# Performance work log

Hardware: AMD Instinct MI355X
Metric: run time of the kernel (lower is better)

## Reference

```python
import jax, jax.numpy as jnp
import numpy as np

C = 128          # inchannel
CH = C // 2      # projected channels
N_, D_, H_, W_ = 2, 16, 16, 16


def setup_inputs() -> dict:
    key = jax.random.key(0)
    kx, kq, kk, kv, kp = jax.random.split(key, 5)
    s_in = 1.0 / np.sqrt(C)
    s_mid = 1.0 / np.sqrt(CH)
    return {
        "x": jax.random.normal(kx, (N_, C, D_, H_, W_), dtype=jnp.float32),
        "Wq": jax.random.normal(kq, (CH, C), dtype=jnp.float32) * s_in,
        "Wk": jax.random.normal(kk, (CH, C), dtype=jnp.float32) * s_in,
        "Wv": jax.random.normal(kv, (CH, C), dtype=jnp.float32) * s_in,
        "Wpost": jax.random.normal(kp, (C, CH), dtype=jnp.float32) * s_mid,
    }


def reference(x, Wq, Wk, Wv, Wpost):
    n, c_in, d, h, w = x.shape
    npos = d * h * w
    xf = x.reshape(n, c_in, npos)                     # (n, C, N)
    # 1x1x1 conv3d (no bias) == channel-mixing matmul
    q = jnp.einsum('oc,ncx->nox', Wq, xf)             # (n, CH, N)
    k = jnp.einsum('oc,ncx->nox', Wk, xf)             # (n, CH, N)
    v = jnp.einsum('oc,ncx->nox', Wv, xf)             # (n, CH, N)
    # atten_map[b,i,j] = sum_c k[b,c,i] * q[b,c,j], softmax over j (dim=2)
    scores = jnp.einsum('nci,ncj->nij', k, q)         # (n, N, N)
    attn = jax.nn.softmax(scores, axis=2)
    # val @ attn: out[b,c,j] = sum_i v[b,c,i] * attn[b,i,j]
    agg = jnp.einsum('nci,nij->ncj', v, attn)         # (n, CH, N)
    post = jnp.einsum('oc,ncx->nox', Wpost, agg)      # (n, C, N)
    return post.reshape(n, c_in, d, h, w) + x
```

## Files before the change

kernel.cpp:

```cpp
#include <hip/hip_runtime.h>
#include <math.h>

#define NB   2
#define CIN  128
#define CH   64
#define NPOS 4096

typedef __attribute__((ext_vector_type(8))) short s16x8;
typedef __attribute__((ext_vector_type(4))) float f32x4;

__device__ __forceinline__ unsigned int bfrne(float f) {
    unsigned int u = __float_as_uint(f);
    return (u + 0x7FFFu + ((u >> 16) & 1u)) >> 16;
}
__device__ __forceinline__ unsigned int pk_rne(float lo, float hi) {
    return bfrne(lo) | (bfrne(hi) << 16);
}
__device__ __forceinline__ unsigned int pk_fast(float lo, float hi) {
    unsigned int a = (__float_as_uint(lo) + 0x8000u) >> 16;
    unsigned int b = (__float_as_uint(hi) + 0x8000u) & 0xFFFF0000u;
    return a | b;
}
__device__ __forceinline__ float bf2f(unsigned short h) {
    return __uint_as_float(((unsigned int)h) << 16);
}

__global__ __launch_bounds__(256) void packw_kernel(
    const float* __restrict__ Wq, const float* __restrict__ Wk,
    const float* __restrict__ Wv, const float* __restrict__ Wpost,
    unsigned short* __restrict__ Wb)
{
    const int gid = blockIdx.x * 256 + threadIdx.x;
    const int base = gid * 4;
    const int mat = base >> 13, off = base & 8191;
    const float* src = (mat == 0) ? Wq : (mat == 1) ? Wk : (mat == 2) ? Wv : Wpost;
    float4 f = *(const float4*)&src[off];
    uint2 st = make_uint2(pk_rne(f.x, f.y), pk_rne(f.z, f.w));
    *(uint2*)&Wb[mat * 8192 + off] = st;
}

#define XTS 132
__global__ __launch_bounds__(256) void qkv_kernel(
    const float* __restrict__ x, const unsigned short* __restrict__ Wb,
    unsigned short* __restrict__ kT, unsigned short* __restrict__ qT,
    float* __restrict__ v32)
{
    __shared__ __align__(16) float xT[16 * XTS];
    const int b  = blockIdx.y;
    const int p0 = blockIdx.x * 16;
    const int tid = threadIdx.x;

    #pragma unroll
    for (int it = 0; it < 2; ++it) {
        int idx = it * 256 + tid;
        int c = idx >> 2, p4 = (idx & 3) * 4;
        float4 g = *(const float4*)&x[((size_t)b * CIN + c) * NPOS + p0 + p4];
        xT[(p4 + 0) * XTS + c] = g.x;
        xT[(p4 + 1) * XTS + c] = g.y;
        xT[(p4 + 2) * XTS + c] = g.z;
        xT[(p4 + 3) * XTS + c] = g.w;
    }
    __syncthreads();

    const int w = tid >> 6, l = tid & 63, lm = l & 15, lq = l >> 4;
    const int p = p0 + lm;

    s16x8 Bhi[4], Blo[4];
    #pragma unroll
    for (int ck = 0; ck < 4; ++ck) {
        const float* xr = &xT[lm * XTS + ck * 32 + lq * 8];
        union { unsigned int u[4]; s16x8 v; } chv, clv;
        #pragma unroll
        for (int j = 0; j < 4; ++j) {
            float x0 = xr[2 * j], x1 = xr[2 * j + 1];
            unsigned int h0 = bfrne(x0), h1 = bfrne(x1);
            chv.u[j] = h0 | (h1 << 16);
            clv.u[j] = pk_rne(x0 - __uint_as_float(h0 << 16),
                              x1 - __uint_as_float(h1 << 16));
        }
        Bhi[ck] = chv.v; Blo[ck] = clv.v;
    }

    #pragma unroll
    for (int t3 = 0; t3 < 3; ++t3) {
        const int tile = w * 3 + t3;
        const int mat = tile >> 2, o0 = (tile & 3) * 16;
        const unsigned short* Wm = Wb + mat * 8192;
        f32x4 acc = {0.f, 0.f, 0.f, 0.f};
        #pragma unroll
        for (int ck = 0; ck < 4; ++ck) {
            s16x8 aW = *(const s16x8*)&Wm[(o0 + lm) * CIN + ck * 32 + lq * 8];
            acc = __builtin_amdgcn_mfma_f32_16x16x32_bf16(aW, Bhi[ck], acc, 0,0,0);
            acc = __builtin_amdgcn_mfma_f32_16x16x32_bf16(aW, Blo[ck], acc, 0,0,0);
        }
        if (mat < 2) {
            unsigned short* dst = (mat == 0) ? qT : kT;
            uint2 st = make_uint2(pk_rne(acc[0], acc[1]), pk_rne(acc[2], acc[3]));
            *(uint2*)&dst[((size_t)b * NPOS + p) * CH + o0 + lq * 4] = st;
        } else {
            #pragma unroll
            for (int r = 0; r < 4; ++r)
                v32[((size_t)b * CH + o0 + lq * 4 + r) * NPOS + p] = acc[r];
        }
    }
}

__global__ __launch_bounds__(256) void stats_kernel(
    const unsigned short* __restrict__ kT,
    const unsigned short* __restrict__ qT,
    float* __restrict__ lpart)
{
    __shared__ __align__(16) unsigned short qbuf[4096];
    const int b  = blockIdx.z;
    const int jq = blockIdx.y;
    const int i0 = blockIdx.x * 128;
    const int tid = threadIdx.x;
    const int w = tid >> 6, l = tid & 63, lm = l & 15, lq = l >> 4;

    s16x8 a[2][2];
    #pragma unroll
    for (int s = 0; s < 2; ++s)
        #pragma unroll
        for (int kc = 0; kc < 2; ++kc)
            a[s][kc] = *(const s16x8*)&kT[
                ((size_t)b * NPOS + i0 + w * 32 + s * 16 + lm) * CH + kc * 32 + lq * 8];

    const unsigned short* qpt =
        qT + ((size_t)b * NPOS + jq * 512 + w * 16 + lm) * CH + lq * 8;
    s16x8 st0 = *(const s16x8*)(qpt);
    s16x8 st1 = *(const s16x8*)(qpt + 32);

    float rs[2][4] = {};
    for (int t = 0; t < 8; ++t) {
        *(s16x8*)&qbuf[(2 * w + 0) * 512 + l * 8] = st0;
        *(s16x8*)&qbuf[(2 * w + 1) * 512 + l * 8] = st1;
        __syncthreads();
        if (t < 7) {
            const unsigned short* qn = qpt + (size_t)(t + 1) * 64 * CH;
            st0 = *(const s16x8*)(qn);
            st1 = *(const s16x8*)(qn + 32);
        }
        #pragma unroll
        for (int js = 0; js < 4; ++js) {
            s16x8 b0 = *(const s16x8*)&qbuf[(js * 2 + 0) * 512 + l * 8];
            s16x8 b1 = *(const s16x8*)&qbuf[(js * 2 + 1) * 512 + l * 8];
            #pragma unroll
            for (int s = 0; s < 2; ++s) {
                f32x4 sc = {0.f, 0.f, 0.f, 0.f};
                sc = __builtin_amdgcn_mfma_f32_16x16x32_bf16(a[s][0], b0, sc, 0,0,0);
                sc = __builtin_amdgcn_mfma_f32_16x16x32_bf16(a[s][1], b1, sc, 0,0,0);
                rs[s][0] += __expf(sc[0]); rs[s][1] += __expf(sc[1]);
                rs[s][2] += __expf(sc[2]); rs[s][3] += __expf(sc[3]);
            }
        }
        __syncthreads();
    }

    #pragma unroll
    for (int s = 0; s < 2; ++s)
        #pragma unroll
        for (int r = 0; r < 4; ++r) {
            #pragma unroll
            for (int m = 1; m < 16; m <<= 1)
                rs[s][r] += __shfl_xor(rs[s][r], m);
        }
    if (lm == 0) {
        #pragma unroll
        for (int s = 0; s < 2; ++s)
            #pragma unroll
            for (int r = 0; r < 4; ++r)
                lpart[(size_t)jq * NB * NPOS + b * NPOS
                      + i0 + w * 32 + s * 16 + lq * 4 + r] = rs[s][r];
    }
}

__global__ __launch_bounds__(256) void combine_kernel(
    const float* __restrict__ lpart, const float* __restrict__ v32,
    unsigned short* __restrict__ vbs)
{
    const int idx4 = blockIdx.x * 256 + threadIdx.x;
    const int base = idx4 * 4;
    const int b = base >> 18;
    const int i = base & (NPOS - 1);
    const float* lp = lpart + b * NPOS + i;
    float sx = 0.f, sy = 0.f, sz = 0.f, sw = 0.f;
    #pragma unroll
    for (int qq = 0; qq < 8; ++qq) {
        float4 lv = *(const float4*)(lp + (size_t)qq * NB * NPOS);
        sx += lv.x; sy += lv.y; sz += lv.z; sw += lv.w;
    }
    float4 v = *(const float4*)&v32[base];
    uint2 st = make_uint2(pk_rne(v.x / sx, v.y / sy),
                          pk_rne(v.z / sz, v.w / sw));
    *(uint2*)&vbs[base] = st;
}

__global__ __launch_bounds__(256) void agg_kernel(
    const unsigned short* __restrict__ kT,
    const unsigned short* __restrict__ qT,
    const unsigned short* __restrict__ vbs,
    unsigned short* __restrict__ U)
{
    __shared__ __align__(16) unsigned short kbuf[2048];
    __shared__ __align__(16) unsigned short vbuf[2048];
    const int b  = blockIdx.z;
    const int iq = blockIdx.y;
    const int j0 = blockIdx.x * 128;
    const int tid = threadIdx.x;
    const int w = tid >> 6, l = tid & 63, lm = l & 15, lq = l >> 4;

    s16x8 qb[2][2];
    #pragma unroll
    for (int js = 0; js < 2; ++js)
        #pragma unroll
        for (int kc = 0; kc < 2; ++kc)
            qb[js][kc] = *(const s16x8*)&qT[
                ((size_t)b * NPOS + j0 + w * 32 + js * 16 + lm) * CH + kc * 32 + lq * 8];

    int addr[4];
    #pragma unroll
    for (int d = 0; d < 4; ++d)
        addr[d] = (lm + 16 * (2 * (lq & 1) + (d >> 1))) << 2;
    const bool lowhalf = (lq < 2);

    const unsigned short* kpt = kT
        + ((size_t)b * NPOS + iq * 512 + (w >> 1) * 16 + lm) * CH
        + (w & 1) * 32 + lq * 8;
    const unsigned short* vpt = vbs
        + ((size_t)b * CH + w * 16 + lm) * NPOS + iq * 512 + lq * 8;

    f32x4 acc[2][4] = {};
    s16x8 kst = *(const s16x8*)kpt;
    s16x8 vst = *(const s16x8*)vpt;

    for (int t = 0; t < 16; ++t) {
        *(s16x8*)&kbuf[w * 512 + l * 8] = kst;
        *(s16x8*)&vbuf[w * 512 + l * 8] = vst;
        __syncthreads();
        if (t < 15) {
            kst = *(const s16x8*)(kpt + (t + 1) * 32 * CH);
            vst = *(const s16x8*)(vpt + (t + 1) * 32);
        }
        s16x8 kA[2][2], vA[4];
        #pragma unroll
        for (int s = 0; s < 2; ++s)
            #pragma unroll
            for (int kc = 0; kc < 2; ++kc)
                kA[s][kc] = *(const s16x8*)&kbuf[(s * 2 + kc) * 512 + l * 8];
        #pragma unroll
        for (int cs = 0; cs < 4; ++cs)
            vA[cs] = *(const s16x8*)&vbuf[cs * 512 + l * 8];

        #pragma unroll
        for (int js = 0; js < 2; ++js) {
            f32x4 s0 = {0,0,0,0}, s1 = {0,0,0,0};
            s0 = __builtin_amdgcn_mfma_f32_16x16x32_bf16(kA[0][0], qb[js][0], s0, 0,0,0);
            s0 = __builtin_amdgcn_mfma_f32_16x16x32_bf16(kA[0][1], qb[js][1], s0, 0,0,0);
            s1 = __builtin_amdgcn_mfma_f32_16x16x32_bf16(kA[1][0], qb[js][0], s1, 0,0,0);
            s1 = __builtin_amdgcn_mfma_f32_16x16x32_bf16(kA[1][1], qb[js][1], s1, 0,0,0);

            unsigned int P0[2], P1[2];
            P0[0] = pk_fast(__expf(s0[0]), __expf(s0[1]));
            P0[1] = pk_fast(__expf(s0[2]), __expf(s0[3]));
            P1[0] = pk_fast(__expf(s1[0]), __expf(s1[1]));
            P1[1] = pk_fast(__expf(s1[2]), __expf(s1[3]));

            union { unsigned int u[4]; s16x8 v; } B;
            #pragma unroll
            for (int d = 0; d < 4; ++d) {
                int t0 = __builtin_amdgcn_ds_bpermute(addr[d], (int)P0[d & 1]);
                int t1 = __builtin_amdgcn_ds_bpermute(addr[d], (int)P1[d & 1]);
                B.u[d] = lowhalf ? (unsigned int)t0 : (unsigned int)t1;
            }
            #pragma unroll
            for (int cs = 0; cs < 4; ++cs)
                acc[js][cs] = __builtin_amdgcn_mfma_f32_16x16x32_bf16(
                    vA[cs], B.v, acc[js][cs], 0,0,0);
        }
        __syncthreads();
    }

    unsigned short* Up = U + ((size_t)iq * NB + b) * NPOS * CH;
    #pragma unroll
    for (int js = 0; js < 2; ++js)
        #pragma unroll
        for (int cs = 0; cs < 4; ++cs) {
            uint2 st = make_uint2(pk_rne(acc[js][cs][0], acc[js][cs][1]),
                                  pk_rne(acc[js][cs][2], acc[js][cs][3]));
            *(uint2*)&Up[(size_t)(j0 + w * 32 + js * 16 + lm) * CH
                         + cs * 16 + lq * 4] = st;
        }
}

__global__ __launch_bounds__(256) void post_kernel(
    const float* __restrict__ x, const unsigned short* __restrict__ Wb,
    const unsigned short* __restrict__ U, float* __restrict__ out)
{
    const int b  = blockIdx.y;
    const int p0 = blockIdx.x * 32;
    const int tid = threadIdx.x;
    const int w = tid >> 6, l = tid & 63, lm = l & 15, lq = l >> 4;
    const int psub = (w & 1) * 16, ohalf = w >> 1;
    const int p = p0 + psub + lm;
    const size_t PS = (size_t)NB * NPOS * CH;

    const unsigned short* u = U + ((size_t)b * NPOS + p) * CH;
    const unsigned short* Wpb = Wb + 3 * 8192;
    s16x8 Bf[2];
    #pragma unroll
    for (int ck = 0; ck < 2; ++ck) {
        float sv[8] = {};
        #pragma unroll
        for (int qq = 0; qq < 8; ++qq) {
            union { s16x8 v; unsigned short us[8]; } uu;
            uu.v = *(const s16x8*)(u + (size_t)qq * PS + ck * 32 + lq * 8);
            #pragma unroll
            for (int j = 0; j < 8; ++j) sv[j] += bf2f(uu.us[j]);
        }
        union { unsigned int u[4]; s16x8 v; } cb;
        #pragma unroll
        for (int j = 0; j < 4; ++j) cb.u[j] = pk_rne(sv[2*j], sv[2*j+1]);
        Bf[ck] = cb.v;
    }

    #pragma unroll
    for (int ot = 0; ot < 4; ++ot) {
        const int o0 = (ohalf * 4 + ot) * 16;
        f32x4 acc = {0.f, 0.f, 0.f, 0.f};
        #pragma unroll
        for (int ck = 0; ck < 2; ++ck) {
            s16x8 aW = *(const s16x8*)&Wpb[(o0 + lm) * CH + ck * 32 + lq * 8];
            acc = __builtin_amdgcn_mfma_f32_16x16x32_bf16(aW, Bf[ck], acc, 0,0,0);
        }
        #pragma unroll
        for (int r = 0; r < 4; ++r) {
            size_t gi = ((size_t)b * CIN + o0 + lq * 4 + r) * NPOS + p;
            out[gi] = x[gi] + acc[r];
        }
    }
}

extern "C" void kernel_launch(void* const* d_in, const int* in_sizes, int n_in,
                              void* d_out, int out_size, void* d_ws, size_t ws_size,
                              hipStream_t stream) {
    const float* x     = (const float*)d_in[0];
    const float* Wq    = (const float*)d_in[1];
    const float* Wk    = (const float*)d_in[2];
    const float* Wv    = (const float*)d_in[3];
    const float* Wpost = (const float*)d_in[4];
    float* out = (float*)d_out;

    unsigned short* kT  = (unsigned short*)d_ws;
    unsigned short* qT  = kT + (size_t)NB * NPOS * CH;
    unsigned short* vbs = qT + (size_t)NB * NPOS * CH;
    unsigned short* Wb  = vbs + (size_t)NB * NPOS * CH;
    float* lpart = (float*)(Wb + 4 * 8192);
    unsigned short* U = (unsigned short*)(lpart + (size_t)8 * NB * NPOS);
    float* v32 = (float*)U;

    packw_kernel  <<<dim3(32), 256, 0, stream>>>(Wq, Wk, Wv, Wpost, Wb);
    qkv_kernel    <<<dim3(NPOS / 16, NB), 256, 0, stream>>>(x, Wb, kT, qT, v32);
    stats_kernel  <<<dim3(NPOS / 128, 8, NB), 256, 0, stream>>>(kT, qT, lpart);
    combine_kernel<<<dim3(NB * CH * NPOS / 1024), 256, 0, stream>>>(lpart, v32, vbs);
    agg_kernel    <<<dim3(NPOS / 128, 8, NB), 256, 0, stream>>>(kT, qT, vbs, U);
    post_kernel   <<<dim3(NPOS / 32, NB), 256, 0, stream>>>(x, Wb, U, out);
}
```

Before: 109.9 us.

## Split kernels into finer grids and double-buffer LDS tiles in attention passes

The change splits every stage into more blocks. qkv gets a third grid axis over output-tile groups, stats uses 64-row key blocks, agg splits the key range into 16 partials instead of 8, and post handles 16 positions and sums 16 partials. The stats and agg loops now use two LDS buffers, so one __syncthreads per iteration can be removed, and launch bounds request 4 blocks per CU. The aim is better occupancy and more blocks across the CUs. In exchange, post reads twice as many partial buffers, the U workspace grows, and qkv recomputes the x transpose once per output group.

Measured after the change: 118.5 us. 7.9% more time.

```diff
diff --git a/kernel.cpp b/kernel.cpp
--- a/kernel.cpp
+++ b/kernel.cpp
@@ -40,13 +40,14 @@
 }
 
 #define XTS 132
-__global__ __launch_bounds__(256) void qkv_kernel(
+__global__ __launch_bounds__(256, 4) void qkv_kernel(
     const float* __restrict__ x, const unsigned short* __restrict__ Wb,
     unsigned short* __restrict__ kT, unsigned short* __restrict__ qT,
     float* __restrict__ v32)
 {
     __shared__ __align__(16) float xT[16 * XTS];
-    const int b  = blockIdx.y;
+    const int b  = blockIdx.z;
+    const int og = blockIdx.y;
     const int p0 = blockIdx.x * 16;
     const int tid = threadIdx.x;
 
@@ -81,96 +82,84 @@
         Bhi[ck] = chv.v; Blo[ck] = clv.v;
     }
 
-    #pragma unroll
-    for (int t3 = 0; t3 < 3; ++t3) {
-        const int tile = w * 3 + t3;
-        const int mat = tile >> 2, o0 = (tile & 3) * 16;
-        const unsigned short* Wm = Wb + mat * 8192;
-        f32x4 acc = {0.f, 0.f, 0.f, 0.f};
-        #pragma unroll
-        for (int ck = 0; ck < 4; ++ck) {
-            s16x8 aW = *(const s16x8*)&Wm[(o0 + lm) * CIN + ck * 32 + lq * 8];
-            acc = __builtin_amdgcn_mfma_f32_16x16x32_bf16(aW, Bhi[ck], acc, 0,0,0);
-            acc = __builtin_amdgcn_mfma_f32_16x16x32_bf16(aW, Blo[ck], acc, 0,0,0);
-        }
-        if (mat < 2) {
-            unsigned short* dst = (mat == 0) ? qT : kT;
-            uint2 st = make_uint2(pk_rne(acc[0], acc[1]), pk_rne(acc[2], acc[3]));
-            *(uint2*)&dst[((size_t)b * NPOS + p) * CH + o0 + lq * 4] = st;
-        } else {
-            #pragma unroll
-            for (int r = 0; r < 4; ++r)
-                v32[((size_t)b * CH + o0 + lq * 4 + r) * NPOS + p] = acc[r];
-        }
-    }
-}
-
-__global__ __launch_bounds__(256) void stats_kernel(
+    const int tile = og * 4 + w;
+    const int mat = tile >> 2, o0 = (tile & 3) * 16;
+    const unsigned short* Wm = Wb + mat * 8192;
+    f32x4 acc = {0.f, 0.f, 0.f, 0.f};
+    #pragma unroll
+    for (int ck = 0; ck < 4; ++ck) {
+        s16x8 aW = *(const s16x8*)&Wm[(o0 + lm) * CIN + ck * 32 + lq * 8];
+        acc = __builtin_amdgcn_mfma_f32_16x16x32_bf16(aW, Bhi[ck], acc, 0,0,0);
+        acc = __builtin_amdgcn_mfma_f32_16x16x32_bf16(aW, Blo[ck], acc, 0,0,0);
+    }
+    if (mat < 2) {
+        unsigned short* dst = (mat == 0) ? qT : kT;
+        uint2 st = make_uint2(pk_rne(acc[0], acc[1]), pk_rne(acc[2], acc[3]));
+        *(uint2*)&dst[((size_t)b * NPOS + p) * CH + o0 + lq * 4] = st;
+    } else {
+        #pragma unroll
+        for (int r = 0; r < 4; ++r)
+            v32[((size_t)b * CH + o0 + lq * 4 + r) * NPOS + p] = acc[r];
+    }
+}
+
+__global__ __launch_bounds__(256, 4) void stats_kernel(
     const unsigned short* __restrict__ kT,
     const unsigned short* __restrict__ qT,
     float* __restrict__ lpart)
 {
-    __shared__ __align__(16) unsigned short qbuf[4096];
+    __shared__ __align__(16) unsigned short qbuf[2][4096];
     const int b  = blockIdx.z;
     const int jq = blockIdx.y;
-    const int i0 = blockIdx.x * 128;
+    const int i0 = blockIdx.x * 64;
     const int tid = threadIdx.x;
     const int w = tid >> 6, l = tid & 63, lm = l & 15, lq = l >> 4;
 
-    s16x8 a[2][2];
-    #pragma unroll
-    for (int s = 0; s < 2; ++s)
-        #pragma unroll
-        for (int kc = 0; kc < 2; ++kc)
-            a[s][kc] = *(const s16x8*)&kT[
-                ((size_t)b * NPOS + i0 + w * 32 + s * 16 + lm) * CH + kc * 32 + lq * 8];
+    s16x8 a0 = *(const s16x8*)&kT[
+        ((size_t)b * NPOS + i0 + w * 16 + lm) * CH + lq * 8];
+    s16x8 a1 = *(const s16x8*)&kT[
+        ((size_t)b * NPOS + i0 + w * 16 + lm) * CH + 32 + lq * 8];
 
     const unsigned short* qpt =
         qT + ((size_t)b * NPOS + jq * 512 + w * 16 + lm) * CH + lq * 8;
     s16x8 st0 = *(const s16x8*)(qpt);
     s16x8 st1 = *(const s16x8*)(qpt + 32);
 
-    float rs[2][4] = {};
+    float rs[4] = {0.f, 0.f, 0.f, 0.f};
     for (int t = 0; t < 8; ++t) {
-        *(s16x8*)&qbuf[(2 * w + 0) * 512 + l * 8] = st0;
-        *(s16x8*)&qbuf[(2 * w + 1) * 512 + l * 8] = st1;
-        __syncthreads();
+        const int buf = t & 1;
+        *(s16x8*)&qbuf[buf][(2 * w + 0) * 512 + l * 8] = st0;
+        *(s16x8*)&qbuf[buf][(2 * w + 1) * 512 + l * 8] = st1;
         if (t < 7) {
             const unsigned short* qn = qpt + (size_t)(t + 1) * 64 * CH;
             st0 = *(const s16x8*)(qn);
             st1 = *(const s16x8*)(qn + 32);
         }
+        __syncthreads();
         #pragma unroll
         for (int js = 0; js < 4; ++js) {
-            s16x8 b0 = *(const s16x8*)&qbuf[(js * 2 + 0) * 512 + l * 8];
-            s16x8 b1 = *(const s16x8*)&qbuf[(js * 2 + 1) * 512 + l * 8];
-            #pragma unroll
-            for (int s = 0; s < 2; ++s) {
-                f32x4 sc = {0.f, 0.f, 0.f, 0.f};
-                sc = __builtin_amdgcn_mfma_f32_16x16x32_bf16(a[s][0], b0, sc, 0,0,0);
-                sc = __builtin_amdgcn_mfma_f32_16x16x32_bf16(a[s][1], b1, sc, 0,0,0);
-                rs[s][0] += __expf(sc[0]); rs[s][1] += __expf(sc[1]);
-                rs[s][2] += __expf(sc[2]); rs[s][3] += __expf(sc[3]);
-            }
-        }
-        __syncthreads();
-    }
-
-    #pragma unroll
-    for (int s = 0; s < 2; ++s)
-        #pragma unroll
-        for (int r = 0; r < 4; ++r) {
-            #pragma unroll
-            for (int m = 1; m < 16; m <<= 1)
-                rs[s][r] += __shfl_xor(rs[s][r], m);
-        }
+            s16x8 b0 = *(const s16x8*)&qbuf[buf][(js * 2 + 0) * 512 + l * 8];
+            s16x8 b1 = *(const s16x8*)&qbuf[buf][(js * 2 + 1) * 512 + l * 8];
+            f32x4 sc = {0.f, 0.f, 0.f, 0.f};
+            sc = __builtin_amdgcn_mfma_f32_16x16x32_bf16(a0, b0, sc, 0,0,0);
+            sc = __builtin_amdgcn_mfma_f32_16x16x32_bf16(a1, b1, sc, 0,0,0);
+            rs[0] += __expf(sc[0]); rs[1] += __expf(sc[1]);
+            rs[2] += __expf(sc[2]); rs[3] += __expf(sc[3]);
+        }
+    }
+
+    #pragma unroll
+    for (int r = 0; r < 4; ++r) {
+        rs[r] += __shfl_xor(rs[r], 1);
+        rs[r] += __shfl_xor(rs[r], 2);
+        rs[r] += __shfl_xor(rs[r], 4);
+        rs[r] += __shfl_xor(rs[r], 8);
+    }
     if (lm == 0) {
         #pragma unroll
-        for (int s = 0; s < 2; ++s)
-            #pragma unroll
-            for (int r = 0; r < 4; ++r)
-                lpart[(size_t)jq * NB * NPOS + b * NPOS
-                      + i0 + w * 32 + s * 16 + lq * 4 + r] = rs[s][r];
+        for (int r = 0; r < 4; ++r)
+            lpart[(size_t)jq * NB * NPOS + b * NPOS
+                  + i0 + w * 16 + lq * 4 + r] = rs[r];
     }
 }
 
@@ -195,14 +184,14 @@
     *(uint2*)&vbs[base] = st;
 }
 
-__global__ __launch_bounds__(256) void agg_kernel(
+__global__ __launch_bounds__(256, 4) void agg_kernel(
     const unsigned short* __restrict__ kT,
     const unsigned short* __restrict__ qT,
     const unsigned short* __restrict__ vbs,
     unsigned short* __restrict__ U)
 {
-    __shared__ __align__(16) unsigned short kbuf[2048];
-    __shared__ __align__(16) unsigned short vbuf[2048];
+    __shared__ __align__(16) unsigned short kbuf[2][2048];
+    __shared__ __align__(16) unsigned short vbuf[2][2048];
     const int b  = blockIdx.z;
     const int iq = blockIdx.y;
     const int j0 = blockIdx.x * 128;
@@ -224,32 +213,34 @@
     const bool lowhalf = (lq < 2);
 
     const unsigned short* kpt = kT
-        + ((size_t)b * NPOS + iq * 512 + (w >> 1) * 16 + lm) * CH
+        + ((size_t)b * NPOS + iq * 256 + (w >> 1) * 16 + lm) * CH
         + (w & 1) * 32 + lq * 8;
     const unsigned short* vpt = vbs
-        + ((size_t)b * CH + w * 16 + lm) * NPOS + iq * 512 + lq * 8;
+        + ((size_t)b * CH + w * 16 + lm) * NPOS + iq * 256 + lq * 8;
 
     f32x4 acc[2][4] = {};
     s16x8 kst = *(const s16x8*)kpt;
     s16x8 vst = *(const s16x8*)vpt;
 
-    for (int t = 0; t < 16; ++t) {
-        *(s16x8*)&kbuf[w * 512 + l * 8] = kst;
-        *(s16x8*)&vbuf[w * 512 + l * 8] = vst;
-        __syncthreads();
-        if (t < 15) {
+    for (int t = 0; t < 8; ++t) {
+        const int buf = t & 1;
+        *(s16x8*)&kbuf[buf][w * 512 + l * 8] = kst;
+        *(s16x8*)&vbuf[buf][w * 512 + l * 8] = vst;
+        if (t < 7) {
             kst = *(const s16x8*)(kpt + (t + 1) * 32 * CH);
             vst = *(const s16x8*)(vpt + (t + 1) * 32);
         }
+        __syncthreads();
+
         s16x8 kA[2][2], vA[4];
         #pragma unroll
         for (int s = 0; s < 2; ++s)
             #pragma unroll
             for (int kc = 0; kc < 2; ++kc)
-                kA[s][kc] = *(const s16x8*)&kbuf[(s * 2 + kc) * 512 + l * 8];
+                kA[s][kc] = *(const s16x8*)&kbuf[buf][(s * 2 + kc) * 512 + l * 8];
         #pragma unroll
         for (int cs = 0; cs < 4; ++cs)
-            vA[cs] = *(const s16x8*)&vbuf[cs * 512 + l * 8];
+            vA[cs] = *(const s16x8*)&vbuf[buf][cs * 512 + l * 8];
 
         #pragma unroll
         for (int js = 0; js < 2; ++js) {
@@ -277,7 +268,6 @@
                 acc[js][cs] = __builtin_amdgcn_mfma_f32_16x16x32_bf16(
                     vA[cs], B.v, acc[js][cs], 0,0,0);
         }
-        __syncthreads();
     }
 
     unsigned short* Up = U + ((size_t)iq * NB + b) * NPOS * CH;
@@ -292,16 +282,15 @@
         }
 }
 
-__global__ __launch_bounds__(256) void post_kernel(
+__global__ __launch_bounds__(256, 4) void post_kernel(
     const float* __restrict__ x, const unsigned short* __restrict__ Wb,
     const unsigned short* __restrict__ U, float* __restrict__ out)
 {
     const int b  = blockIdx.y;
-    const int p0 = blockIdx.x * 32;
+    const int p0 = blockIdx.x * 16;
     const int tid = threadIdx.x;
     const int w = tid >> 6, l = tid & 63, lm = l & 15, lq = l >> 4;
-    const int psub = (w & 1) * 16, ohalf = w >> 1;
-    const int p = p0 + psub + lm;
+    const int p = p0 + lm;
     const size_t PS = (size_t)NB * NPOS * CH;
 
     const unsigned short* u = U + ((size_t)b * NPOS + p) * CH;
@@ -311,7 +300,7 @@
     for (int ck = 0; ck < 2; ++ck) {
         float sv[8] = {};
         #pragma unroll
-        for (int qq = 0; qq < 8; ++qq) {
+        for (int qq = 0; qq < 16; ++qq) {
             union { s16x8 v; unsigned short us[8]; } uu;
             uu.v = *(const s16x8*)(u + (size_t)qq * PS + ck * 32 + lq * 8);
             #pragma unroll
@@ -324,8 +313,8 @@
     }
 
     #pragma unroll
-    for (int ot = 0; ot < 4; ++ot) {
-        const int o0 = (ohalf * 4 + ot) * 16;
+    for (int ot = 0; ot < 2; ++ot) {
+        const int o0 = (w * 2 + ot) * 16;
         f32x4 acc = {0.f, 0.f, 0.f, 0.f};
         #pragma unroll
         for (int ck = 0; ck < 2; ++ck) {
@@ -359,9 +348,9 @@
     float* v32 = (float*)U;
 
     packw_kernel  <<<dim3(32), 256, 0, stream>>>(Wq, Wk, Wv, Wpost, Wb);
-    qkv_kernel    <<<dim3(NPOS / 16, NB), 256, 0, stream>>>(x, Wb, kT, qT, v32);
-    stats_kernel  <<<dim3(NPOS / 128, 8, NB), 256, 0, stream>>>(kT, qT, lpart);
+    qkv_kernel    <<<dim3(NPOS / 16, 3, NB), 256, 0, stream>>>(x, Wb, kT, qT, v32);
+    stats_kernel  <<<dim3(NPOS / 64, 8, NB), 256, 0, stream>>>(kT, qT, lpart);
     combine_kernel<<<dim3(NB * CH * NPOS / 1024), 256, 0, stream>>>(lpart, v32, vbs);
-    agg_kernel    <<<dim3(NPOS / 128, 8, NB), 256, 0, stream>>>(kT, qT, vbs, U);
-    post_kernel   <<<dim3(NPOS / 32, NB), 256, 0, stream>>>(x, Wb, U, out);
-}
+    agg_kernel    <<<dim3(NPOS / 128, 16, NB), 256, 0, stream>>>(kT, qT, vbs, U);
+    post_kernel   <<<dim3(NPOS / 16, NB), 256, 0, stream>>>(x, Wb, U, out);
+}
```
